# Kernel optimization log

Measured on AMD Instinct MI355X. Metric: run time of the kernel, lower is better.

Reference implementation:

```python
import jax, jax.numpy as jnp
import numpy as np

N_NODES = 50000
N_FEAT = 256
HIDDEN = 256
N_EDGES = 800000


def gcn_conv(x, edge_index, W, b):
    """PyG GCNConv: out = D^-1/2 (A+I) D^-1/2 (x @ W) + b."""
    n = x.shape[0]
    loop = jnp.arange(n, dtype=edge_index.dtype)
    src = jnp.concatenate([edge_index[0], loop])  # [E+N]
    dst = jnp.concatenate([edge_index[1], loop])  # [E+N]
    deg = jax.ops.segment_sum(jnp.ones_like(dst, dtype=x.dtype), dst, num_segments=n)
    dinv = jnp.where(deg > 0, jax.lax.rsqrt(deg), 0.0)
    norm = dinv[src] * dinv[dst]                  # [E+N]
    h = x @ W                                     # [N, out]
    msg = h[src] * norm[:, None]                  # gather + scale
    out = jax.ops.segment_sum(msg, dst, num_segments=n)  # scatter-add
    return out + b


def setup_inputs() -> dict:
    key = jax.random.key(0)
    ks = jax.random.split(key, 8)
    x = jax.random.normal(ks[0], (N_NODES, N_FEAT), dtype=jnp.float32)
    train_pos_edge_index = jax.random.randint(ks[1], (2, N_EDGES), 0, N_NODES, dtype=jnp.int64)
    pos_edge_index = jax.random.randint(ks[2], (2, N_EDGES), 0, N_NODES, dtype=jnp.int64)
    neg_edge_index = jax.random.randint(ks[3], (2, N_EDGES), 0, N_NODES, dtype=jnp.int64)
    # Glorot-style init for GCN weights
    W1 = jax.random.normal(ks[4], (N_FEAT, HIDDEN), dtype=jnp.float32) * (1.0 / np.sqrt(N_FEAT))
    b1 = jnp.zeros((HIDDEN,), dtype=jnp.float32)
    W2 = jax.random.normal(ks[5], (HIDDEN, HIDDEN // 2), dtype=jnp.float32) * (1.0 / np.sqrt(HIDDEN))
    b2 = jnp.zeros((HIDDEN // 2,), dtype=jnp.float32)
    return {"x": x, "train_pos_edge_index": train_pos_edge_index,
            "pos_edge_index": pos_edge_index, "neg_edge_index": neg_edge_index,
            "W1": W1, "b1": b1, "W2": W2, "b2": b2}


def reference(x, train_pos_edge_index, pos_edge_index, neg_edge_index, W1, b1, W2, b2):
    # encode
    h = jax.nn.relu(gcn_conv(x, train_pos_edge_index, W1, b1))
    z = gcn_conv(h, train_pos_edge_index, W2, b2)  # [N, HIDDEN//2]
    # decode: dot product over concatenated pos+neg edges
    edge_index = jnp.concatenate([pos_edge_index, neg_edge_index], axis=-1)  # [2, 2E]
    logits = jnp.sum(z[edge_index[0]] * z[edge_index[1]], axis=-1)           # [2E]
    return logits
```

## Files before the change

kernel.cpp:

```cpp
#include <hip/hip_runtime.h>
#include <hip/hip_fp16.h>


#define NFEAT 256
#define HID   256
#define OUTF  128

typedef _Float16 f16x8 __attribute__((ext_vector_type(8)));
typedef float    f32x4 __attribute__((ext_vector_type(4)));

__global__ void k_init_deg(float* __restrict__ deg, int n) {
    int i = blockIdx.x * blockDim.x + threadIdx.x;
    if (i < n) deg[i] = 1.0f;
}

__global__ void k_count_deg(const int* __restrict__ ei, float* __restrict__ deg, int E) {
    int e = blockIdx.x * blockDim.x + threadIdx.x;
    if (e < E) atomicAdd(&deg[ei[E + e]], 1.0f);
}

__global__ __launch_bounds__(1024) void k_scan1(
        const float* __restrict__ deg, int* __restrict__ excl,
        int* __restrict__ bsum, int n) {
    __shared__ int swsum[16];
    const int t = threadIdx.x, wave = t >> 6, lane = t & 63;
    const int i = blockIdx.x * 1024 + t;
    int v = (i < n) ? (int)deg[i] - 1 : 0;
    int sc = v;
#pragma unroll
    for (int off = 1; off < 64; off <<= 1) {
        int y = __shfl_up(sc, off);
        if (lane >= off) sc += y;
    }
    if (lane == 63) swsum[wave] = sc;
    __syncthreads();
    if (t < 16) {
        int w = swsum[t];
        int scw = w;
#pragma unroll
        for (int off = 1; off < 16; off <<= 1) {
            int y = __shfl_up(scw, off);
            if (t >= off) scw += y;
        }
        swsum[t] = scw - w;
        if (t == 15) bsum[blockIdx.x] = scw;
    }
    __syncthreads();
    if (i < n) excl[i] = swsum[wave] + (sc - v);
}

__global__ void k_scan2(int* __restrict__ bsum, int nb) {
    int t = threadIdx.x;
    int v = (t < nb) ? bsum[t] : 0;
    int sc = v;
#pragma unroll
    for (int off = 1; off < 64; off <<= 1) {
        int y = __shfl_up(sc, off);
        if (t >= off) sc += y;
    }
    if (t < nb) bsum[t] = sc - v;
    if (t == 63) bsum[nb] = sc;
}

__global__ void k_scan3(float* __restrict__ deg_dinv, const int* __restrict__ excl,
                        const int* __restrict__ bsum, int* __restrict__ rowptr,
                        int* __restrict__ cursor, int n, int nb) {
    int i = blockIdx.x * blockDim.x + threadIdx.x;
    if (i < n) {
        int rp = excl[i] + bsum[i >> 10];
        rowptr[i] = rp;
        cursor[i] = rp;
        deg_dinv[i] = rsqrtf(deg_dinv[i]);
    } else if (i == n) {
        rowptr[n] = bsum[nb];
    }
}

__global__ void k_fill(const int* __restrict__ ei, int* __restrict__ cursor,
                       int* __restrict__ eidx, int E) {
    int e = blockIdx.x * blockDim.x + threadIdx.x;
    if (e < E) {
        int s = ei[e];
        int d = ei[E + e];
        int p = atomicAdd(&cursor[d], 1);
        eidx[p] = s;
    }
}

__global__ __launch_bounds__(256) void k_wt(const float* __restrict__ W,
                                            __half* __restrict__ Wt, int K, int M) {
    __shared__ float tile[32][33];
    int k0 = blockIdx.x * 32, m0 = blockIdx.y * 32;
    int tx = threadIdx.x & 31, ty = threadIdx.x >> 5;
#pragma unroll
    for (int r = 0; r < 4; ++r)
        tile[ty + r * 8][tx] = W[(size_t)(k0 + ty + r * 8) * M + m0 + tx];
    __syncthreads();
#pragma unroll
    for (int r = 0; r < 4; ++r)
        Wt[(size_t)(m0 + ty + r * 8) * K + k0 + tx] = __float2half(tile[tx][ty + r * 8]);
}

template <int MT, bool AF32, int SWL>
__global__ __launch_bounds__(256) void k_gemm_mfma(
        const void* __restrict__ Aptr, const __half* __restrict__ Wt,
        const float* __restrict__ dinv, __half* __restrict__ outp,
        int n, int K, int M) {
    constexpr int BM = 2 * MT * 16;
    __shared__ __half As[BM][40];
    __shared__ __half Bs[128][40];
    __shared__ __half Cs[4][16][72];

    const int t    = threadIdx.x;
    const int wave = t >> 6;
    const int lane = t & 63;
    const int row0 = blockIdx.x * BM;
    const int col0 = blockIdx.y * 128;
    const int wm = wave >> 1, wn = wave & 1;
    const int lr = lane & 15;
    const int kq = lane >> 4;

    f32x4 acc[MT][4];
#pragma unroll
    for (int i = 0; i < MT; ++i)
#pragma unroll
        for (int j = 0; j < 4; ++j) acc[i][j] = (f32x4){0.f, 0.f, 0.f, 0.f};

    for (int k0 = 0; k0 < K; k0 += 32) {
        if (AF32) {
            const float* A = (const float*)Aptr;
#pragma unroll
            for (int it = 0; it < BM * 8 / 256; ++it) {
                int q = t + it * 256;
                int r = q >> 3, c4 = q & 7;
                int gr = min(row0 + r, n - 1);
                float4 v = *(const float4*)&A[(size_t)gr * K + k0 + c4 * 4];
                __half2* dst = (__half2*)&As[r][c4 * 4];
                dst[0] = __floats2half2_rn(v.x, v.y);
                dst[1] = __floats2half2_rn(v.z, v.w);
            }
        } else {
            const __half* A = (const __half*)Aptr;
#pragma unroll
            for (int it = 0; it < BM * 4 / 256; ++it) {
                int q = t + it * 256;
                int r = q >> 2, c8 = q & 3;
                int gr = min(row0 + r, n - 1);
                *(float4*)&As[r][c8 * 8] = *(const float4*)&A[(size_t)gr * K + k0 + c8 * 8];
            }
        }
#pragma unroll
        for (int it = 0; it < 2; ++it) {
            int q = t + it * 256;
            int r = q >> 2, c8 = q & 3;
            *(float4*)&Bs[r][c8 * 8] = *(const float4*)&Wt[(size_t)(col0 + r) * K + k0 + c8 * 8];
        }
        __syncthreads();

        f16x8 b[4];
#pragma unroll
        for (int j = 0; j < 4; ++j)
            b[j] = *(const f16x8*)&Bs[wn * 64 + j * 16 + lr][kq * 8];
#pragma unroll
        for (int i = 0; i < MT; ++i) {
            f16x8 a = *(const f16x8*)&As[wm * MT * 16 + i * 16 + lr][kq * 8];
#pragma unroll
            for (int j = 0; j < 4; ++j)
                acc[i][j] = __builtin_amdgcn_mfma_f32_16x16x32_f16(a, b[j], acc[i][j], 0, 0, 0);
        }
        __syncthreads();
    }

    constexpr int SW = 1 << SWL;
#pragma unroll
    for (int i = 0; i < MT; ++i) {
        int gr0 = row0 + wm * MT * 16 + i * 16;
        float dv[4];
#pragma unroll
        for (int r = 0; r < 4; ++r)
            dv[r] = dinv[min(gr0 + kq * 4 + r, n - 1)];
        __syncthreads();
#pragma unroll
        for (int j = 0; j < 4; ++j)
#pragma unroll
            for (int r = 0; r < 4; ++r)
                Cs[wave][kq * 4 + r][j * 16 + lr] = __float2half(acc[i][j][r] * dv[r]);
        __syncthreads();
        int r1 = lane >> 3, c1 = (lane & 7) * 8;
#pragma unroll
        for (int h = 0; h < 2; ++h) {
            int grow = gr0 + r1 + h * 8;
            if (grow < n) {
                int col = col0 + wn * 64 + c1;
                size_t oidx = ((size_t)(col >> SWL) * n + grow) * SW + (col & (SW - 1));
                *(float4*)&outp[oidx] = *(const float4*)&Cs[wave][r1 + h * 8][c1];
            }
        }
    }
}

__global__ __launch_bounds__(256) void k_agg1(
        const int* __restrict__ rowptr, const int* __restrict__ eidx,
        const __half* __restrict__ g, const float* __restrict__ dinv,
        const float* __restrict__ bias, __half* __restrict__ out, int n) {
    const int node = (int)(((size_t)blockIdx.x * blockDim.x + threadIdx.x) >> 6);
    const int lane = threadIdx.x & 63;
    const int half = lane >> 5;
    const int fl   = lane & 31;
    if (node >= n) return;
    const int j0  = rowptr[node];
    const int end = rowptr[node + 1];
    const int last = end - 1;

    union U { float4 f; __half2 h[4]; };
    float acc[8] = {0.f, 0.f, 0.f, 0.f, 0.f, 0.f, 0.f, 0.f};
    {
        if (half == 0) {
            U u; u.f = *(const float4*)&g[(size_t)node * HID + fl * 8];
#pragma unroll
            for (int k = 0; k < 4; ++k) {
                float2 v = __half22float2(u.h[k]);
                acc[k * 2] += v.x; acc[k * 2 + 1] += v.y;
            }
        }
    }
    if (j0 < end) {
        int s0 = eidx[min(j0 + half, last)];
        int s1 = eidx[min(j0 + 2 + half, last)];
        for (int j = j0; j < end; j += 4) {
            int p0 = eidx[min(j + 4 + half, last)];
            int p1 = eidx[min(j + 6 + half, last)];
            U u0, u1;
            u0.f = *(const float4*)&g[(size_t)s0 * HID + fl * 8];
            u1.f = *(const float4*)&g[(size_t)s1 * HID + fl * 8];
            if (j + half < end) {
#pragma unroll
                for (int k = 0; k < 4; ++k) {
                    float2 v = __half22float2(u0.h[k]);
                    acc[k * 2] += v.x; acc[k * 2 + 1] += v.y;
                }
            }
            if (j + 2 + half < end) {
#pragma unroll
                for (int k = 0; k < 4; ++k) {
                    float2 v = __half22float2(u1.h[k]);
                    acc[k * 2] += v.x; acc[k * 2 + 1] += v.y;
                }
            }
            s0 = p0; s1 = p1;
        }
    }
#pragma unroll
    for (int k = 0; k < 8; ++k) acc[k] += __shfl_xor(acc[k], 32);
    if (half == 0) {
        const float sc = dinv[node];
        const int f0 = fl * 8;
        U r;
#pragma unroll
        for (int k = 0; k < 4; ++k) {
            float2 bb = *(const float2*)&bias[f0 + k * 2];
            r.h[k] = __floats2half2_rn(fmaxf(sc * acc[k * 2]     + bb.x, 0.f),
                                       fmaxf(sc * acc[k * 2 + 1] + bb.y, 0.f));
        }
        *(float4*)&out[(size_t)node * HID + f0] = r.f;
    }
}

__global__ __launch_bounds__(256) void k_agg2(
        const int* __restrict__ rowptr, const int* __restrict__ eidx,
        const __half* __restrict__ g, const float* __restrict__ dinv,
        const float* __restrict__ bias, __half* __restrict__ out, int n) {
    const int node = (int)(((size_t)blockIdx.x * blockDim.x + threadIdx.x) >> 6);
    const int lane = threadIdx.x & 63;
    const int q    = lane >> 4;
    const int fl   = lane & 15;
    if (node >= n) return;
    const int j0  = rowptr[node];
    const int end = rowptr[node + 1];
    const int last = end - 1;

    union U { float4 f; __half2 h[4]; };
    float acc[8] = {0.f, 0.f, 0.f, 0.f, 0.f, 0.f, 0.f, 0.f};
    if (q == 0) {
        U u; u.f = *(const float4*)&g[(size_t)node * OUTF + fl * 8];
#pragma unroll
        for (int k = 0; k < 4; ++k) {
            float2 v = __half22float2(u.h[k]);
            acc[k * 2] += v.x; acc[k * 2 + 1] += v.y;
        }
    }
    if (j0 < end) {
        int s0 = eidx[min(j0 + q, last)];
        for (int j = j0; j < end; j += 4) {
            int p0 = eidx[min(j + 4 + q, last)];
            U u0; u0.f = *(const float4*)&g[(size_t)s0 * OUTF + fl * 8];
            if (j + q < end) {
#pragma unroll
                for (int k = 0; k < 4; ++k) {
                    float2 v = __half22float2(u0.h[k]);
                    acc[k * 2] += v.x; acc[k * 2 + 1] += v.y;
                }
            }
            s0 = p0;
        }
    }
#pragma unroll
    for (int k = 0; k < 8; ++k) {
        acc[k] += __shfl_xor(acc[k], 16);
        acc[k] += __shfl_xor(acc[k], 32);
    }
    if (q == 0) {
        const float sc = dinv[node];
        const int f0 = fl * 8;
        U r;
#pragma unroll
        for (int k = 0; k < 4; ++k) {
            float2 bb = *(const float2*)&bias[f0 + k * 2];
            r.h[k] = __floats2half2_rn(sc * acc[k * 2]     + bb.x,
                                       sc * acc[k * 2 + 1] + bb.y);
        }
        *(float4*)&out[(size_t)node * OUTF + f0] = r.f;
    }
}

__global__ void k_decode(const int* __restrict__ pos, const int* __restrict__ neg,
                         const __half* __restrict__ z, float* __restrict__ out, int E) {
    size_t gid = (size_t)blockIdx.x * blockDim.x + threadIdx.x;
    int e  = (int)(gid >> 4);
    int sl = (int)(threadIdx.x & 15);
    if (e >= 2 * E) return;
    int a, b;
    if (e < E) { a = pos[e];     b = pos[E + e]; }
    else       { a = neg[e - E]; b = neg[e];     }
    union HF4 { float4 f; __half2 h[4]; };
    HF4 ua, ub;
    ua.f = ((const float4*)(z + (size_t)a * OUTF))[sl];
    ub.f = ((const float4*)(z + (size_t)b * OUTF))[sl];
    float p = 0.f;
#pragma unroll
    for (int k = 0; k < 4; ++k) {
        float2 fa = __half22float2(ua.h[k]);
        float2 fb = __half22float2(ub.h[k]);
        p = fmaf(fa.x, fb.x, p);
        p = fmaf(fa.y, fb.y, p);
    }
    p += __shfl_xor(p, 1);
    p += __shfl_xor(p, 2);
    p += __shfl_xor(p, 4);
    p += __shfl_xor(p, 8);
    if (sl == 0) out[e] = p;
}

extern "C" void kernel_launch(void* const* d_in, const int* in_sizes, int n_in,
                              void* d_out, int out_size, void* d_ws, size_t ws_size,
                              hipStream_t stream) {
    const float* x   = (const float*)d_in[0];
    const int*   tei = (const int*)d_in[1];
    const int*   pos = (const int*)d_in[2];
    const int*   neg = (const int*)d_in[3];
    const float* W1  = (const float*)d_in[4];
    const float* b1  = (const float*)d_in[5];
    const float* W2  = (const float*)d_in[6];
    const float* b2  = (const float*)d_in[7];
    float* out = (float*)d_out;

    const int N = in_sizes[0] / NFEAT;
    const int E = in_sizes[1] / 2;
    const int NB = (N + 1023) / 1024;

    char* ws = (char*)d_ws;
    size_t off = 0;
    __half* g1h = (__half*)(ws + off);
    __half* g2h = (__half*)(ws + off);
    __half* zh  = (__half*)(ws + off + (size_t)N * OUTF * 2);
    off += (size_t)N * HID * 2;
    __half* h1h = (__half*)(ws + off);  off += (size_t)N * HID * 2;
    float*  dinv = (float*)(ws + off);  off += (size_t)N * 4;
    int* rowptr = (int*)(ws + off);     off += (size_t)(N + 1) * 4;
    int* cursor = (int*)(ws + off);     off += (size_t)N * 4;
    int* eidx   = (int*)(ws + off);     off += (size_t)E * 4;
    __half* W1t = (__half*)(ws + off);  off += (size_t)NFEAT * HID * 2;
    __half* W2t = (__half*)(ws + off);  off += (size_t)HID * OUTF * 2;
    int* excl   = (int*)(ws + off);     off += (size_t)N * 4;
    int* bsum   = (int*)(ws + off);     off += (size_t)(NB + 1) * 4;

    { dim3 g(NFEAT / 32, HID / 32);  k_wt<<<g, 256, 0, stream>>>(W1, W1t, NFEAT, HID); }
    { dim3 g(HID / 32, OUTF / 32);   k_wt<<<g, 256, 0, stream>>>(W2, W2t, HID, OUTF); }

    k_init_deg<<<(N + 255) / 256, 256, 0, stream>>>(dinv, N);
    k_count_deg<<<(E + 255) / 256, 256, 0, stream>>>(tei, dinv, E);
    k_scan1<<<NB, 1024, 0, stream>>>(dinv, excl, bsum, N);
    k_scan2<<<1, 64, 0, stream>>>(bsum, NB);
    k_scan3<<<(N + 256) / 256, 256, 0, stream>>>(dinv, excl, bsum, rowptr, cursor, N, NB);
    k_fill<<<(E + 255) / 256, 256, 0, stream>>>(tei, cursor, eidx, E);

    {
        dim3 grid((N + 127) / 128, HID / 128);
        k_gemm_mfma<4, true, 8><<<grid, 256, 0, stream>>>(x, W1t, dinv, g1h, N, NFEAT, HID);
        int nblk = (int)(((size_t)N * 64 + 255) / 256);
        k_agg1<<<nblk, 256, 0, stream>>>(rowptr, eidx, g1h, dinv, b1, h1h, N);
    }

    {
        dim3 grid((N + 63) / 64, OUTF / 128);
        k_gemm_mfma<2, false, 7><<<grid, 256, 0, stream>>>(h1h, W2t, dinv, g2h, N, HID, OUTF);
        int nblk = (int)(((size_t)N * 64 + 255) / 256);
        k_agg2<<<nblk, 256, 0, stream>>>(rowptr, eidx, g2h, dinv, b2, zh, N);
    }

    {
        size_t nth = (size_t)2 * E * 16;
        k_decode<<<(int)((nth + 255) / 256), 256, 0, stream>>>(pos, neg, zh, out, E);
    }
}
```

Before: 429.4 us.

## Split z into feature slices and decode per slice with fdot2 plus reduction

The output of agg2 is stored as four 32-feature slices ([4][N][32]) instead of row-major [N][128]. The decode kernel now handles one slice per block, so the gather working set per pass is a quarter of z and is more likely to stay in cache. Each edge uses two lanes with fdot2, and the partial sums go to a buffer. A new k_dsum kernel adds the four partials. This trades an extra launch, extra index reloads per slice and a partial-sum write and read for better cache locality of the random z gathers.

```diff
diff --git a/kernel.cpp b/kernel.cpp
--- a/kernel.cpp
+++ b/kernel.cpp
@@ -7,6 +7,7 @@
 #define OUTF  128
 
 typedef _Float16 f16x8 __attribute__((ext_vector_type(8)));
+typedef _Float16 f16x2 __attribute__((ext_vector_type(2)));
 typedef float    f32x4 __attribute__((ext_vector_type(4)));
 
 __global__ void k_init_deg(float* __restrict__ deg, int n) {
@@ -269,7 +270,7 @@
 __global__ __launch_bounds__(256) void k_agg2(
         const int* __restrict__ rowptr, const int* __restrict__ eidx,
         const __half* __restrict__ g, const float* __restrict__ dinv,
-        const float* __restrict__ bias, __half* __restrict__ out, int n) {
+        const float* __restrict__ bias, __half* __restrict__ zs, int n) {
     const int node = (int)(((size_t)blockIdx.x * blockDim.x + threadIdx.x) >> 6);
     const int lane = threadIdx.x & 63;
     const int q    = lane >> 4;
@@ -319,36 +320,58 @@
             r.h[k] = __floats2half2_rn(sc * acc[k * 2]     + bb.x,
                                        sc * acc[k * 2 + 1] + bb.y);
         }
-        *(float4*)&out[(size_t)node * OUTF + f0] = r.f;
-    }
-}
-
-__global__ void k_decode(const int* __restrict__ pos, const int* __restrict__ neg,
-                         const __half* __restrict__ z, float* __restrict__ out, int E) {
-    size_t gid = (size_t)blockIdx.x * blockDim.x + threadIdx.x;
-    int e  = (int)(gid >> 4);
-    int sl = (int)(threadIdx.x & 15);
+        *(float4*)&zs[((size_t)(f0 >> 5) * n + node) * 32 + (f0 & 31)] = r.f;
+    }
+}
+
+__global__ __launch_bounds__(256) void k_decode(
+        const int* __restrict__ pos, const int* __restrict__ neg,
+        const __half* __restrict__ zs, float* __restrict__ psum, int E, int n) {
+    const int slice = blockIdx.x & 3;
+    const int wv    = threadIdx.x >> 6;
+    const int lane  = threadIdx.x & 63;
+    const int eo    = lane >> 1;
+    const int h     = lane & 1;
+    int e = ((blockIdx.x >> 2) * 4 + wv) * 32 + eo;
     if (e >= 2 * E) return;
     int a, b;
     if (e < E) { a = pos[e];     b = pos[E + e]; }
     else       { a = neg[e - E]; b = neg[e];     }
-    union HF4 { float4 f; __half2 h[4]; };
-    HF4 ua, ub;
-    ua.f = ((const float4*)(z + (size_t)a * OUTF))[sl];
-    ub.f = ((const float4*)(z + (size_t)b * OUTF))[sl];
+    const __half* ra = zs + ((size_t)slice * n + a) * 32 + h * 16;
+    const __half* rb = zs + ((size_t)slice * n + b) * 32 + h * 16;
+    union U { float4 f; f16x2 d[4]; };
+    U a0, a1, b0, b1;
+    a0.f = *(const float4*)&ra[0];
+    a1.f = *(const float4*)&ra[8];
+    b0.f = *(const float4*)&rb[0];
+    b1.f = *(const float4*)&rb[8];
     float p = 0.f;
+#if __has_builtin(__builtin_amdgcn_fdot2)
+#pragma unroll
+    for (int k = 0; k < 4; ++k) p = __builtin_amdgcn_fdot2(a0.d[k], b0.d[k], p, false);
+#pragma unroll
+    for (int k = 0; k < 4; ++k) p = __builtin_amdgcn_fdot2(a1.d[k], b1.d[k], p, false);
+#else
 #pragma unroll
     for (int k = 0; k < 4; ++k) {
-        float2 fa = __half22float2(ua.h[k]);
-        float2 fb = __half22float2(ub.h[k]);
-        p = fmaf(fa.x, fb.x, p);
-        p = fmaf(fa.y, fb.y, p);
-    }
+        p += (float)a0.d[k][0] * (float)b0.d[k][0] + (float)a0.d[k][1] * (float)b0.d[k][1];
+        p += (float)a1.d[k][0] * (float)b1.d[k][0] + (float)a1.d[k][1] * (float)b1.d[k][1];
+    }
+#endif
     p += __shfl_xor(p, 1);
-    p += __shfl_xor(p, 2);
-    p += __shfl_xor(p, 4);
-    p += __shfl_xor(p, 8);
-    if (sl == 0) out[e] = p;
+    if (h == 0)
+        __builtin_nontemporal_store(p, &psum[(size_t)slice * 2 * E + e]);
+}
+
+__global__ void k_dsum(const float* __restrict__ psum, float* __restrict__ out, int n2e) {
+    int e = blockIdx.x * blockDim.x + threadIdx.x;
+    if (e < n2e) {
+        float p0 = __builtin_nontemporal_load(&psum[e]);
+        float p1 = __builtin_nontemporal_load(&psum[(size_t)n2e + e]);
+        float p2 = __builtin_nontemporal_load(&psum[2 * (size_t)n2e + e]);
+        float p3 = __builtin_nontemporal_load(&psum[3 * (size_t)n2e + e]);
+        out[e] = (p0 + p1) + (p2 + p3);
+    }
 }
 
 extern "C" void kernel_launch(void* const* d_in, const int* in_sizes, int n_in,
@@ -372,9 +395,11 @@
     size_t off = 0;
     __half* g1h = (__half*)(ws + off);
     __half* g2h = (__half*)(ws + off);
-    __half* zh  = (__half*)(ws + off + (size_t)N * OUTF * 2);
+    __half* zs  = (__half*)(ws + off + (size_t)N * OUTF * 2);
     off += (size_t)N * HID * 2;
-    __half* h1h = (__half*)(ws + off);  off += (size_t)N * HID * 2;
+    __half* h1h  = (__half*)(ws + off);
+    float*  psum = (float*)(ws + off);
+    off += (size_t)N * HID * 2;
     float*  dinv = (float*)(ws + off);  off += (size_t)N * 4;
     int* rowptr = (int*)(ws + off);     off += (size_t)(N + 1) * 4;
     int* cursor = (int*)(ws + off);     off += (size_t)N * 4;
@@ -405,11 +430,12 @@
         dim3 grid((N + 63) / 64, OUTF / 128);
         k_gemm_mfma<2, false, 7><<<grid, 256, 0, stream>>>(h1h, W2t, dinv, g2h, N, HID, OUTF);
         int nblk = (int)(((size_t)N * 64 + 255) / 256);
-        k_agg2<<<nblk, 256, 0, stream>>>(rowptr, eidx, g2h, dinv, b2, zh, N);
+        k_agg2<<<nblk, 256, 0, stream>>>(rowptr, eidx, g2h, dinv, b2, zs, N);
     }
 
     {
-        size_t nth = (size_t)2 * E * 16;
-        k_decode<<<(int)((nth + 255) / 256), 256, 0, stream>>>(pos, neg, zh, out, E);
-    }
-}
+        int nblk = 4 * ((2 * E + 127) / 128);
+        k_decode<<<nblk, 256, 0, stream>>>(pos, neg, zs, psum, E, N);
+        k_dsum<<<(2 * E + 255) / 256, 256, 0, stream>>>(psum, out, 2 * E);
+    }
+}
```

Measured after the change: 406.8 us. -5.3%, faster.
